# Kernel optimization log

Hardware: AMD Instinct MI355X
Metric: run time of the kernel (lower is better)

## Reference

```python
import jax, jax.numpy as jnp
import numpy as np

E = 8          # num_experts
K = 2          # top_k
CAP_FACTOR = 1.0


def setup_inputs() -> dict:
    key = jax.random.key(0)
    ks = jax.random.split(key, 5)
    B, T, C, H = 4, 2048, 1024, 4096
    x = jax.random.normal(ks[0], (B, T, C), dtype=jnp.float32)
    Wr = jax.random.normal(ks[1], (C, E), dtype=jnp.float32) * 0.02
    br = jnp.zeros((E,), jnp.float32)
    W1 = jax.random.normal(ks[2], (E, C, H), dtype=jnp.float32) * 0.02
    b1 = jnp.zeros((E, H), jnp.float32)
    W2 = jax.random.normal(ks[3], (E, H, C), dtype=jnp.float32) * 0.02
    b2 = jnp.zeros((E, C), jnp.float32)
    return {"x": x, "Wr": Wr, "br": br, "W1": W1, "b1": b1, "W2": W2, "b2": b2}


def reference(x, Wr, br, W1, b1, W2, b2):
    B, T, C = x.shape
    N = B * T
    xf = x.reshape(N, C)

    # ---- router: top-k over logits, softmax over selected logits (eval: no noise) ----
    logits = xf @ Wr + br                          # [N, E]
    topv, topi = jax.lax.top_k(logits, K)          # [N, K]
    gates = jax.nn.softmax(topv, axis=-1)          # [N, K]
    rw = jnp.zeros((N, E), xf.dtype).at[jnp.arange(N)[:, None], topi].set(gates)  # [N, E]

    # ---- capacity-limited dispatch (tokens kept in ascending token order, like torch.nonzero) ----
    cap = int(N * K / E * CAP_FACTOR)
    sel = jax.nn.one_hot(topi, E, dtype=jnp.int32).sum(1)   # [N, E] 0/1
    rank = jnp.cumsum(sel, axis=0) - sel                    # position among this expert's tokens
    keep = (sel > 0) & (rank < cap)
    tok = jnp.broadcast_to(jnp.arange(N, dtype=jnp.int32)[:, None], (N, E))
    eid = jnp.broadcast_to(jnp.arange(E, dtype=jnp.int32)[None, :], (N, E))
    rank_c = jnp.where(keep, rank, cap)                     # dropped slots go out of bounds
    buf = jnp.full((E, cap), N, dtype=jnp.int32)            # N = padding token id
    buf = buf.at[eid, rank_c].set(tok, mode='drop')         # [E, cap]

    # ---- gather -> per-expert FFN (grouped GEMM) -> weighted scatter-add ----
    xpad = jnp.concatenate([xf, jnp.zeros((1, C), xf.dtype)], axis=0)
    xg = xpad[buf]                                          # [E, cap, C]
    h = jax.nn.gelu(jnp.einsum('ecd,edh->ech', xg, W1) + b1[:, None, :], approximate=False)
    out = jnp.einsum('ech,ehd->ecd', h, W2) + b2[:, None, :]  # [E, cap, C]
    rw_pad = jnp.concatenate([rw, jnp.zeros((1, E), rw.dtype)], axis=0)
    w = rw_pad[buf, jnp.arange(E, dtype=jnp.int32)[:, None]]  # [E, cap]
    weighted = out * w[..., None]
    final = jnp.zeros((N + 1, C), xf.dtype).at[buf.reshape(-1)].add(weighted.reshape(-1, C))
    return final[:N].reshape(B, T, C)
```

## Files before the change

kernel.cpp:

```cpp
#include <hip/hip_runtime.h>
#include <hip/hip_bf16.h>

#define E_NUM 8
#define KSEL 2

typedef __attribute__((ext_vector_type(8))) short short8;
typedef __attribute__((ext_vector_type(4))) float f32x4;

__device__ inline unsigned short f2bf(float f) {
  unsigned int u = __float_as_uint(f);
  unsigned int lsb = (u >> 16) & 1u;
  u += 0x7fffu + lsb;
  return (unsigned short)(u >> 16);
}

__device__ inline void gload16(const unsigned short* g, unsigned short* l) {
  __builtin_amdgcn_global_load_lds(
      (const __attribute__((address_space(1))) unsigned int*)(const void*)g,
      (__attribute__((address_space(3))) unsigned int*)(void*)l, 16, 0, 0);
}

__global__ __launch_bounds__(256) void cvt_bf16_kernel(const float* __restrict__ in,
                                                       unsigned short* __restrict__ out,
                                                       long n) {
  long i = ((long)blockIdx.x * 256 + threadIdx.x) * 8;
  if (i >= n) return;
  float4 a = *(const float4*)(in + i);
  float4 b = *(const float4*)(in + i + 4);
  union { unsigned short us[8]; uint4 v; } u;
  u.us[0] = f2bf(a.x); u.us[1] = f2bf(a.y); u.us[2] = f2bf(a.z); u.us[3] = f2bf(a.w);
  u.us[4] = f2bf(b.x); u.us[5] = f2bf(b.y); u.us[6] = f2bf(b.z); u.us[7] = f2bf(b.w);
  *(uint4*)(out + i) = u.v;
}

__global__ __launch_bounds__(256) void router_kernel(
    const float* __restrict__ x, const float* __restrict__ Wr, const float* __restrict__ br,
    int N, int C,
    int* __restrict__ top1, int* __restrict__ top2,
    float* __restrict__ g1, float* __restrict__ g2) {
  int wave = threadIdx.x >> 6;
  int lane = threadIdx.x & 63;
  int n = blockIdx.x * 4 + wave;
  if (n >= N) return;
  float acc[E_NUM];
#pragma unroll
  for (int e = 0; e < E_NUM; ++e) acc[e] = 0.f;
  const float* xr = x + (long)n * C;
  for (int c = lane; c < C; c += 64) {
    float xv = xr[c];
    const float* wr = Wr + (long)c * E_NUM;
    float4 w0 = *(const float4*)(wr);
    float4 w1 = *(const float4*)(wr + 4);
    acc[0] += xv * w0.x; acc[1] += xv * w0.y; acc[2] += xv * w0.z; acc[3] += xv * w0.w;
    acc[4] += xv * w1.x; acc[5] += xv * w1.y; acc[6] += xv * w1.z; acc[7] += xv * w1.w;
  }
#pragma unroll
  for (int off = 32; off > 0; off >>= 1)
#pragma unroll
    for (int e = 0; e < E_NUM; ++e) acc[e] += __shfl_xor(acc[e], off, 64);
  if (lane == 0) {
    float v1 = -3.4e38f, v2 = -3.4e38f; int i1 = 0, i2 = 0;
#pragma unroll
    for (int e = 0; e < E_NUM; ++e) {
      float v = acc[e] + br[e];
      if (v > v1) { v2 = v1; i2 = i1; v1 = v; i1 = e; }
      else if (v > v2) { v2 = v; i2 = e; }
    }
    float t = expf(v2 - v1);
    float s = 1.f / (1.f + t);
    top1[n] = i1; top2[n] = i2;
    g1[n] = s;    g2[n] = t * s;
  }
}

__global__ __launch_bounds__(1024) void scan_kernel(
    const int* __restrict__ top1, const int* __restrict__ top2,
    const float* __restrict__ g1, const float* __restrict__ g2,
    int N, int cap, int* __restrict__ buf, float* __restrict__ wgt) {
  const int e = blockIdx.x;
  const int t = threadIdx.x;
  const int TP = N / 1024;
  __shared__ int sc[1024];
  int sel[8]; float gv[8];
  int tot = 0;
  const int base_n = t * TP;
#pragma unroll
  for (int i = 0; i < 8; ++i) {
    if (i >= TP) break;
    int n = base_n + i;
    int s1 = (top1[n] == e);
    int s2 = (top2[n] == e);
    sel[i] = s1 | s2;
    gv[i] = s1 ? g1[n] : g2[n];
    tot += sel[i];
  }
  sc[t] = tot;
  __syncthreads();
  for (int off = 1; off < 1024; off <<= 1) {
    int v = (t >= off) ? sc[t - off] : 0;
    __syncthreads();
    sc[t] += v;
    __syncthreads();
  }
  int base = sc[t] - tot;
  int count = sc[1023];
#pragma unroll
  for (int i = 0; i < 8; ++i) {
    if (i >= TP) break;
    if (sel[i]) {
      if (base < cap) {
        buf[e * cap + base] = base_n + i;
        wgt[e * cap + base] = gv[i];
      }
      ++base;
    }
  }
  for (int s = count + t; s < cap; s += 1024) {
    buf[e * cap + s] = N;
    wgt[e * cap + s] = 0.f;
  }
}

__global__ __launch_bounds__(256) void transpose_kernel(
    const float* __restrict__ in, unsigned short* __restrict__ out,
    int R, int S, long strideIn, long strideOut, int eGlobal) {
  __shared__ float tile[64][65];
  const float* src = in + (long)(eGlobal + blockIdx.z) * strideIn;
  unsigned short* dst = out + (long)blockIdx.z * strideOut;
  int s0 = blockIdx.x * 64, r0 = blockIdx.y * 64;
  int t = threadIdx.x;
  int rl = t >> 4, sl = (t & 15) * 4;
#pragma unroll
  for (int rr = 0; rr < 4; ++rr) {
    int r = rl + rr * 16;
    float4 v = *(const float4*)(src + (long)(r0 + r) * S + s0 + sl);
    tile[r][sl] = v.x; tile[r][sl + 1] = v.y; tile[r][sl + 2] = v.z; tile[r][sl + 3] = v.w;
  }
  __syncthreads();
#pragma unroll
  for (int it = 0; it < 2; ++it) {
    int idx = t + it * 256;
    int so = idx >> 3;
    int rc = (idx & 7) * 8;
    union { unsigned short us[8]; uint4 v; } u;
#pragma unroll
    for (int j = 0; j < 8; ++j) u.us[j] = f2bf(tile[rc + j][so]);
    *(uint4*)(dst + (long)(s0 + so) * R + r0 + rc) = u.v;
  }
}

template <int MODE>
__global__ __launch_bounds__(256) void moe_gemm(
    const unsigned short* __restrict__ A, const unsigned short* __restrict__ B,
    const int* __restrict__ buf, const float* __restrict__ wgt,
    const float* __restrict__ bias, const unsigned short* __restrict__ zp,
    unsigned short* __restrict__ Hout, float* __restrict__ Fout,
    int Kdim, int Nn, int cap, int Ntok,
    int eGlobal, long strideB, long strideH) {
  const int tid = threadIdx.x;
  const int lane = tid & 63;
  const int wave = tid >> 6;
  const int wr = wave >> 1, wc = wave & 1;
  const int eIdx = blockIdx.z;
  const int expert = eGlobal + eIdx;
  const int m0 = blockIdx.y * 128;
  const int n0 = blockIdx.x * 128;

  const unsigned short* Bexp = B + (long)eIdx * strideB;

  __shared__ unsigned short As[128 * 64];
  __shared__ unsigned short Bs[128 * 64];

  const unsigned short* aRow[4];
  const unsigned short* bRow[4];
  int aStep[4];
#pragma unroll
  for (int q = 0; q < 4; ++q) {
    int idx = tid + q * 256;
    int r = idx >> 3;
    int cOff = ((((idx & 7) << 4) ^ ((r & 7) << 4)) >> 1);
    if (MODE == 0) {
      int tok = buf[expert * cap + m0 + r];
      bool ok = (tok < Ntok);
      aRow[q] = ok ? (A + (long)tok * Kdim + cOff) : (zp + cOff);
      aStep[q] = ok ? 64 : 0;
    } else {
      aRow[q] = A + (long)eIdx * strideH + (long)(m0 + r) * Kdim + cOff;
      aStep[q] = 64;
    }
    bRow[q] = Bexp + (long)(n0 + r) * Kdim + cOff;
  }

  f32x4 acc[4][4];
#pragma unroll
  for (int i = 0; i < 4; ++i)
#pragma unroll
    for (int j = 0; j < 4; ++j) acc[i][j] = {0.f, 0.f, 0.f, 0.f};

  const int rA = lane & 15;
  const int kByte = (lane >> 4) * 16;
  const int wbase = wave * 64 * 8;

  for (int kt = 0; kt < Kdim; kt += 64) {
#pragma unroll
    for (int q = 0; q < 4; ++q) {
      gload16(aRow[q], As + wbase + q * 2048);
      gload16(bRow[q], Bs + wbase + q * 2048);
      aRow[q] += aStep[q];
      bRow[q] += 64;
    }
    __syncthreads();
#pragma unroll
    for (int ks = 0; ks < 2; ++ks) {
      short8 af[4], bg[4];
#pragma unroll
      for (int mi = 0; mi < 4; ++mi) {
        int row = wr * 64 + mi * 16 + rA;
        int o = row * 128 + ks * 64 + kByte;
        o ^= (row & 7) << 4;
        af[mi] = *(const short8*)((const char*)As + o);
      }
#pragma unroll
      for (int ni = 0; ni < 4; ++ni) {
        int row = wc * 64 + ni * 16 + rA;
        int o = row * 128 + ks * 64 + kByte;
        o ^= (row & 7) << 4;
        bg[ni] = *(const short8*)((const char*)Bs + o);
      }
#pragma unroll
      for (int mi = 0; mi < 4; ++mi)
#pragma unroll
        for (int ni = 0; ni < 4; ++ni)
          acc[mi][ni] = __builtin_amdgcn_mfma_f32_16x16x32_bf16(af[mi], bg[ni], acc[mi][ni], 0, 0, 0);
    }
    __syncthreads();
  }

  if (MODE == 0) {
    const float* b1 = bias + (long)expert * Nn;
    unsigned short* hExp = Hout + (long)eIdx * strideH;
#pragma unroll
    for (int ni = 0; ni < 4; ++ni) {
      int col = n0 + wc * 64 + ni * 16 + (lane & 15);
      float bv = b1[col];
#pragma unroll
      for (int mi = 0; mi < 4; ++mi) {
        int row0 = m0 + wr * 64 + mi * 16 + (lane >> 4) * 4;
#pragma unroll
        for (int r = 0; r < 4; ++r) {
          float v = acc[mi][ni][r] + bv;
          float gl = 0.5f * v * (1.f + erff(v * 0.70710678118654752f));
          hExp[(long)(row0 + r) * Nn + col] = f2bf(gl);
        }
      }
    }
  } else {
    const float* b2 = bias + (long)expert * Nn;
#pragma unroll
    for (int mi = 0; mi < 4; ++mi) {
      int row0 = m0 + wr * 64 + mi * 16 + (lane >> 4) * 4;
#pragma unroll
      for (int r = 0; r < 4; ++r) {
        int slot = row0 + r;
        int tok = buf[expert * cap + slot];
        if (tok >= Ntok) continue;
        float w = wgt[expert * cap + slot];
#pragma unroll
        for (int ni = 0; ni < 4; ++ni) {
          int col = n0 + wc * 64 + ni * 16 + (lane & 15);
          float v = (acc[mi][ni][r] + b2[col]) * w;
          unsafeAtomicAdd(Fout + (long)tok * Nn + col, v);
        }
      }
    }
  }
}

extern "C" void kernel_launch(void* const* d_in, const int* in_sizes, int n_in,
                              void* d_out, int out_size, void* d_ws, size_t ws_size,
                              hipStream_t stream) {
  const float* x  = (const float*)d_in[0];
  const float* Wr = (const float*)d_in[1];
  const float* br = (const float*)d_in[2];
  const float* W1 = (const float*)d_in[3];
  const float* b1 = (const float*)d_in[4];
  const float* W2 = (const float*)d_in[5];
  const float* b2 = (const float*)d_in[6];
  float* out = (float*)d_out;

  const int C = in_sizes[1] / E_NUM;
  const long NC = in_sizes[0];
  const int N = (int)(NC / C);
  const int H = in_sizes[4] / E_NUM;
  const int cap = N * KSEL / E_NUM;

  char* p = (char*)d_ws;
  auto alloc = [&](size_t bytes) { char* r = p; p += (bytes + 255) & ~255ULL; return r; };

  unsigned short* xb = (unsigned short*)alloc((size_t)N * C * 2);
  int*   top1 = (int*)alloc((size_t)N * 4);
  int*   top2 = (int*)alloc((size_t)N * 4);
  float* g1   = (float*)alloc((size_t)N * 4);
  float* g2   = (float*)alloc((size_t)N * 4);
  int*   buf  = (int*)alloc((size_t)E_NUM * cap * 4);
  float* wgt  = (float*)alloc((size_t)E_NUM * cap * 4);
  unsigned short* zp = (unsigned short*)alloc(256);
  size_t commonBytes = (size_t)(p - (char*)d_ws);

  const size_t w1tFull = (size_t)E_NUM * C * H * 2;
  const size_t w2tFull = (size_t)E_NUM * H * C * 2;
  const size_t hFull   = (size_t)E_NUM * cap * H * 2;
  const bool full = ws_size >= commonBytes + w1tFull + w2tFull + hFull + 4096;

  hipMemsetAsync(d_out, 0, (size_t)out_size * sizeof(float), stream);
  hipMemsetAsync(zp, 0, 256, stream);
  cvt_bf16_kernel<<<(int)(((long)N * C) / (256 * 8)), 256, 0, stream>>>(x, xb, (long)N * C);
  router_kernel<<<(N + 3) / 4, 256, 0, stream>>>(x, Wr, br, N, C, top1, top2, g1, g2);
  scan_kernel<<<E_NUM, 1024, 0, stream>>>(top1, top2, g1, g2, N, cap, buf, wgt);

  if (full) {
    unsigned short* W1T = (unsigned short*)alloc(w1tFull);
    unsigned short* W2T = (unsigned short*)alloc(w2tFull);
    unsigned short* hb  = (unsigned short*)alloc(hFull);
    transpose_kernel<<<dim3(H / 64, C / 64, E_NUM), 256, 0, stream>>>(
        W1, W1T, C, H, (long)C * H, (long)C * H, 0);
    moe_gemm<0><<<dim3(H / 128, cap / 128, E_NUM), 256, 0, stream>>>(
        xb, W1T, buf, wgt, b1, zp, hb, nullptr, C, H, cap, N, 0, (long)C * H, (long)cap * H);
    transpose_kernel<<<dim3(C / 64, H / 64, E_NUM), 256, 0, stream>>>(
        W2, W2T, H, C, (long)H * C, (long)H * C, 0);
    moe_gemm<1><<<dim3(C / 128, cap / 128, E_NUM), 256, 0, stream>>>(
        hb, W2T, buf, wgt, b2, zp, nullptr, out, H, C, cap, N, 0, (long)H * C, (long)cap * H);
  } else {
    unsigned short* w1t = (unsigned short*)alloc((size_t)C * H * 2);
    unsigned short* w2t = (unsigned short*)alloc((size_t)H * C * 2);
    unsigned short* hb  = (unsigned short*)alloc((size_t)cap * H * 2);
    for (int e = 0; e < E_NUM; ++e) {
      transpose_kernel<<<dim3(H / 64, C / 64, 1), 256, 0, stream>>>(
          W1, w1t, C, H, (long)C * H, 0, e);
      moe_gemm<0><<<dim3(H / 128, cap / 128, 1), 256, 0, stream>>>(
          xb, w1t, buf, wgt, b1, zp, hb, nullptr, C, H, cap, N, e, 0, 0);
      transpose_kernel<<<dim3(C / 64, H / 64, 1), 256, 0, stream>>>(
          W2, w2t, H, C, (long)H * C, 0, e);
      moe_gemm<1><<<dim3(C / 128, cap / 128, 1), 256, 0, stream>>>(
          hb, w2t, buf, wgt, b2, zp, nullptr, out, H, C, cap, N, e, 0, 0);
    }
  }
}
```

Before: 909.6 us.

## Double-buffer GEMM LDS tiles, remap blocks per XCD, and use tanh-GELU

The grouped GEMM now uses two LDS buffers, so the global-to-LDS load of the next K tile is issued before the MFMA work on the current tile. The 3D grid becomes a 1D grid with a remapping that places consecutive logical tiles of the same expert on the same XCD, meant to improve L2 reuse of weights. The exact erf GELU is replaced by a sigmoid form of the tanh approximation, which is cheaper but changes numerics slightly. Doubling LDS to 64 KB per block may lower occupancy.

```diff
diff --git a/kernel.cpp b/kernel.cpp
--- a/kernel.cpp
+++ b/kernel.cpp
@@ -156,20 +156,32 @@
     const float* __restrict__ bias, const unsigned short* __restrict__ zp,
     unsigned short* __restrict__ Hout, float* __restrict__ Fout,
     int Kdim, int Nn, int cap, int Ntok,
-    int eGlobal, long strideB, long strideH) {
+    int eGlobal, long strideB, long strideH, int nx, int ny) {
   const int tid = threadIdx.x;
   const int lane = tid & 63;
   const int wave = tid >> 6;
   const int wr = wave >> 1, wc = wave & 1;
-  const int eIdx = blockIdx.z;
+
+  const int nwg = gridDim.x;
+  int hw = blockIdx.x;
+  int logical = hw;
+  if ((nwg & 7) == 0) {
+    int cpx = nwg >> 3;
+    logical = (hw & 7) * cpx + (hw >> 3);
+  }
+  const int bPerE = nx * ny;
+  const int eIdx = logical / bPerE;
+  const int rem = logical - eIdx * bPerE;
+  const int bx = rem / ny;
+  const int by = rem - bx * ny;
   const int expert = eGlobal + eIdx;
-  const int m0 = blockIdx.y * 128;
-  const int n0 = blockIdx.x * 128;
+  const int m0 = by * 128;
+  const int n0 = bx * 128;
 
   const unsigned short* Bexp = B + (long)eIdx * strideB;
 
-  __shared__ unsigned short As[128 * 64];
-  __shared__ unsigned short Bs[128 * 64];
+  __shared__ unsigned short As[2][128 * 64];
+  __shared__ unsigned short Bs[2][128 * 64];
 
   const unsigned short* aRow[4];
   const unsigned short* bRow[4];
@@ -191,6 +203,17 @@
     bRow[q] = Bexp + (long)(n0 + r) * Kdim + cOff;
   }
 
+  const int wbase = wave * 64 * 8;
+  auto stage = [&](int b) {
+#pragma unroll
+    for (int q = 0; q < 4; ++q) {
+      gload16(aRow[q], &As[b][wbase + q * 2048]);
+      gload16(bRow[q], &Bs[b][wbase + q * 2048]);
+      aRow[q] += aStep[q];
+      bRow[q] += 64;
+    }
+  };
+
   f32x4 acc[4][4];
 #pragma unroll
   for (int i = 0; i < 4; ++i)
@@ -199,33 +222,30 @@
 
   const int rA = lane & 15;
   const int kByte = (lane >> 4) * 16;
-  const int wbase = wave * 64 * 8;
-
-  for (int kt = 0; kt < Kdim; kt += 64) {
-#pragma unroll
-    for (int q = 0; q < 4; ++q) {
-      gload16(aRow[q], As + wbase + q * 2048);
-      gload16(bRow[q], Bs + wbase + q * 2048);
-      aRow[q] += aStep[q];
-      bRow[q] += 64;
-    }
-    __syncthreads();
+
+  stage(0);
+  __syncthreads();
+
+  const int nk = Kdim >> 6;
+  for (int kt = 0; kt < nk; ++kt) {
+    const int cur = kt & 1;
+    if (kt + 1 < nk) stage(cur ^ 1);
+    const char* aBase = (const char*)As[cur];
+    const char* bBase = (const char*)Bs[cur];
 #pragma unroll
     for (int ks = 0; ks < 2; ++ks) {
       short8 af[4], bg[4];
 #pragma unroll
       for (int mi = 0; mi < 4; ++mi) {
         int row = wr * 64 + mi * 16 + rA;
-        int o = row * 128 + ks * 64 + kByte;
-        o ^= (row & 7) << 4;
-        af[mi] = *(const short8*)((const char*)As + o);
+        int o = (row * 128 + ks * 64 + kByte) ^ ((row & 7) << 4);
+        af[mi] = *(const short8*)(aBase + o);
       }
 #pragma unroll
       for (int ni = 0; ni < 4; ++ni) {
         int row = wc * 64 + ni * 16 + rA;
-        int o = row * 128 + ks * 64 + kByte;
-        o ^= (row & 7) << 4;
-        bg[ni] = *(const short8*)((const char*)Bs + o);
+        int o = (row * 128 + ks * 64 + kByte) ^ ((row & 7) << 4);
+        bg[ni] = *(const short8*)(bBase + o);
       }
 #pragma unroll
       for (int mi = 0; mi < 4; ++mi)
@@ -249,7 +269,7 @@
 #pragma unroll
         for (int r = 0; r < 4; ++r) {
           float v = acc[mi][ni][r] + bv;
-          float gl = 0.5f * v * (1.f + erff(v * 0.70710678118654752f));
+          float gl = v / (1.f + __expf(-1.595769122f * (v + 0.044715f * v * v * v)));
           hExp[(long)(row0 + r) * Nn + col] = f2bf(gl);
         }
       }
@@ -324,12 +344,20 @@
     unsigned short* hb  = (unsigned short*)alloc(hFull);
     transpose_kernel<<<dim3(H / 64, C / 64, E_NUM), 256, 0, stream>>>(
         W1, W1T, C, H, (long)C * H, (long)C * H, 0);
-    moe_gemm<0><<<dim3(H / 128, cap / 128, E_NUM), 256, 0, stream>>>(
-        xb, W1T, buf, wgt, b1, zp, hb, nullptr, C, H, cap, N, 0, (long)C * H, (long)cap * H);
+    {
+      int nx = H / 128, ny = cap / 128;
+      moe_gemm<0><<<nx * ny * E_NUM, 256, 0, stream>>>(
+          xb, W1T, buf, wgt, b1, zp, hb, nullptr, C, H, cap, N, 0,
+          (long)C * H, (long)cap * H, nx, ny);
+    }
     transpose_kernel<<<dim3(C / 64, H / 64, E_NUM), 256, 0, stream>>>(
         W2, W2T, H, C, (long)H * C, (long)H * C, 0);
-    moe_gemm<1><<<dim3(C / 128, cap / 128, E_NUM), 256, 0, stream>>>(
-        hb, W2T, buf, wgt, b2, zp, nullptr, out, H, C, cap, N, 0, (long)H * C, (long)cap * H);
+    {
+      int nx = C / 128, ny = cap / 128;
+      moe_gemm<1><<<nx * ny * E_NUM, 256, 0, stream>>>(
+          hb, W2T, buf, wgt, b2, zp, nullptr, out, H, C, cap, N, 0,
+          (long)H * C, (long)cap * H, nx, ny);
+    }
   } else {
     unsigned short* w1t = (unsigned short*)alloc((size_t)C * H * 2);
     unsigned short* w2t = (unsigned short*)alloc((size_t)H * C * 2);
@@ -337,12 +365,18 @@
     for (int e = 0; e < E_NUM; ++e) {
       transpose_kernel<<<dim3(H / 64, C / 64, 1), 256, 0, stream>>>(
           W1, w1t, C, H, (long)C * H, 0, e);
-      moe_gemm<0><<<dim3(H / 128, cap / 128, 1), 256, 0, stream>>>(
-          xb, w1t, buf, wgt, b1, zp, hb, nullptr, C, H, cap, N, e, 0, 0);
+      {
+        int nx = H / 128, ny = cap / 128;
+        moe_gemm<0><<<nx * ny, 256, 0, stream>>>(
+            xb, w1t, buf, wgt, b1, zp, hb, nullptr, C, H, cap, N, e, 0, 0, nx, ny);
+      }
       transpose_kernel<<<dim3(C / 64, H / 64, 1), 256, 0, stream>>>(
           W2, w2t, H, C, (long)H * C, 0, e);
-      moe_gemm<1><<<dim3(C / 128, cap / 128, 1), 256, 0, stream>>>(
-          hb, w2t, buf, wgt, b2, zp, nullptr, out, H, C, cap, N, e, 0, 0);
-    }
-  }
-}
+      {
+        int nx = C / 128, ny = cap / 128;
+        moe_gemm<1><<<nx * ny, 256, 0, stream>>>(
+            hb, w2t, buf, wgt, b2, zp, nullptr, out, H, C, cap, N, e, 0, 0, nx, ny);
+      }
+    }
+  }
+}
```

After: 851.1 us. -6.4%, faster.
